# Kernel optimization log

Hardware: AMD Instinct MI355X
Metric: run time of the kernel (lower is better)

The kernel has to match this reference:

```python
import jax, jax.numpy as jnp
import numpy as np
import math

S = 128
EPS = 1e-05

def _rope_seq(x):
    # x: [B, L, 2, s]; rope over dim=1 (sequence), matching torch rope(x, dim=1)
    B, L, two, s = x.shape
    half = s // 2
    pos = jnp.arange(L, dtype=jnp.float32)[:, None]              # [L,1] (one unsqueeze)
    inv_freq = 10000.0 ** (jnp.arange(half, dtype=jnp.float32) / half)
    sinusoid = pos[..., None] * inv_freq[None, None, :]          # [L,1,half]
    sin = jnp.sin(sinusoid)
    cos = jnp.cos(sinusoid)
    x1, x2 = jnp.split(x, 2, axis=-1)
    return jnp.concatenate([x1 * cos - x2 * sin, x2 * cos + x1 * sin], axis=-1)

def setup_inputs() -> dict:
    key = jax.random.key(0)
    ks = jax.random.split(key, 8)
    B, L, D = 8, 1024, 1024
    E = 2 * D
    x = jax.random.normal(ks[0], (B, L, D), dtype=jnp.float32)
    g = jnp.ones((1,), dtype=jnp.float32)
    uv_w = jax.random.normal(ks[1], (2 * E + S, D), dtype=jnp.float32) * 0.02
    gamma = jax.random.uniform(ks[2], (2, S), dtype=jnp.float32)
    beta = jax.random.uniform(ks[3], (2, S), dtype=jnp.float32)
    w_rel = jax.random.uniform(ks[4], (2 * L - 1,), dtype=jnp.float32)
    o_w = jax.random.normal(ks[5], (D, E), dtype=jnp.float32) * 0.02
    res_scale = jnp.ones((D,), dtype=jnp.float32)
    return {"x": x, "g": g, "uv_w": uv_w, "gamma": gamma, "beta": beta,
            "w_rel": w_rel, "o_w": o_w, "res_scale": res_scale}

def reference(x, g, uv_w, gamma, beta, w_rel, o_w, res_scale):
    B, L, D = x.shape
    E = (uv_w.shape[0] - S) // 2
    sqrt_s = math.sqrt(S)
    # ScaleNorm
    norm = jnp.linalg.norm(x, axis=-1, keepdims=True) * (D ** -0.5)
    xn = x / jnp.maximum(norm, EPS) * g
    # gated projection + activation
    uv = jax.nn.silu(xn @ uv_w.T)                               # [B,L,2E+S]
    u = uv[..., :E]
    v = uv[..., E:2 * E]
    base = uv[..., 2 * E:]                                       # [B,L,S]
    base = base[:, :, None, :] * gamma[None, None] + beta        # [B,L,2,S]
    base = _rope_seq(base)
    q = base[:, :, 0]                                            # [B,L,S]
    k = base[:, :, 1]
    qk = jnp.einsum('bis,bjs->bij', q, k)                        # [B,L,L]
    # Toeplitz relative bias: bias[i,j] = w_rel[j - i + L - 1]
    idx = jnp.arange(L)[None, :] - jnp.arange(L)[:, None] + (L - 1)
    qk = qk + w_rel[idx][None]
    kernel = jnp.square(jax.nn.relu(qk / sqrt_s))
    out = u * jnp.einsum('bij,bje->bie', kernel, v)              # [B,L,E]
    out = out @ o_w.T                                            # [B,L,D]
    return x * res_scale + out
```

## Files before the change

### kernel.cpp

```cpp
#include <hip/hip_runtime.h>
#include <hip/hip_bf16.h>
#include <math.h>


typedef __hip_bfloat16 bf16;
using v8s = __attribute__((ext_vector_type(8))) short;
using v4f = __attribute__((ext_vector_type(4))) float;
typedef unsigned short u16;

#define BTCH 8
#define LSEQ 1024
#define DDIM 1024
#define EDIM 2048
#define SDIM 128
#define UVN  4224
#define SLABW 4096
#define BUFW  (4 * SLABW)

__device__ __forceinline__ float ldany(const void* p, size_t i, int bf) {
  return bf ? __bfloat162float(((const bf16*)p)[i]) : ((const float*)p)[i];
}
__device__ __forceinline__ void stany(void* p, size_t i, float v, int bf) {
  if (bf) ((bf16*)p)[i] = __float2bfloat16(v);
  else    ((float*)p)[i] = v;
}
__device__ __forceinline__ u16 f2bf(float x) {
  bf16 b = __float2bfloat16(x);
  return *reinterpret_cast<u16*>(&b);
}
__device__ __forceinline__ float bf2f(u16 u) {
  return __uint_as_float((unsigned)u << 16);
}
__device__ __forceinline__ float silu(float v) {
  return v / (1.0f + __expf(-v));
}

__device__ __forceinline__ void xcd_swz(int& bx, int& by) {
  const int W = gridDim.x;
  const int G = W * gridDim.y;
  const int orig = blockIdx.y * W + blockIdx.x;
  const int nid = (orig & 7) * (G >> 3) + (orig >> 3);
  bx = nid % W;
  by = nid / W;
}

__device__ __forceinline__ void gld16(const u16* g, u16* l) {
  __builtin_amdgcn_global_load_lds(
      (const __attribute__((address_space(1))) void*)g,
      (__attribute__((address_space(3))) void*)l, 16, 0, 0);
}

__device__ __forceinline__ const v8s* swz_rd(const u16* slab, int row, int q) {
  return (const v8s*)(slab + row * 32 + ((q ^ ((row >> 1) & 3)) << 3));
}

__global__ void detect_kernel(const u16* g16, int* flag) {
  *flag = (g16[0] == 0x3F80) ? 1 : 0;
}

__global__ __launch_bounds__(256) void wsplit_kernel(const void* __restrict__ w,
                                                     u16* __restrict__ whi,
                                                     u16* __restrict__ wlo,
                                                     const int* __restrict__ flagp,
                                                     int n) {
  const int bf = *flagp;
  const size_t i = ((size_t)blockIdx.x * 256 + threadIdx.x) * 8;
  if (i >= (size_t)n) return;
  if (bf) {
    *(uint4*)(whi + i) = *(const uint4*)((const u16*)w + i);
  } else {
    const float* wf = (const float*)w;
    float t[8];
    *(float4*)&t[0] = *(const float4*)(wf + i);
    *(float4*)&t[4] = *(const float4*)(wf + i + 4);
    u16 h[8], l[8];
    #pragma unroll
    for (int j = 0; j < 8; j++) {
      h[j] = f2bf(t[j]);
      l[j] = f2bf(t[j] - bf2f(h[j]));
    }
    *(uint4*)(whi + i) = *(uint4*)&h[0];
    *(uint4*)(wlo + i) = *(uint4*)&l[0];
  }
}

__global__ __launch_bounds__(256) void rmsnorm_kernel(const void* __restrict__ x,
                                                      const void* __restrict__ g,
                                                      u16* __restrict__ xnhi,
                                                      u16* __restrict__ xnlo,
                                                      const int* __restrict__ flagp,
                                                      unsigned long long row0) {
  const int bf = *flagp;
  const int m = blockIdx.x;
  const size_t gbase = (row0 + m) * DDIM;
  float ss = 0.f;
  float vals[4];
  #pragma unroll
  for (int i = 0; i < 4; i++) {
    vals[i] = ldany(x, gbase + threadIdx.x + i * 256, bf);
    ss += vals[i] * vals[i];
  }
  #pragma unroll
  for (int o = 32; o > 0; o >>= 1) ss += __shfl_down(ss, o);
  __shared__ float red[5];
  if ((threadIdx.x & 63) == 0) red[threadIdx.x >> 6] = ss;
  __syncthreads();
  if (threadIdx.x == 0) {
    float tot = red[0] + red[1] + red[2] + red[3];
    float rms = sqrtf(tot * (1.0f / DDIM));
    red[4] = ldany(g, 0, bf) / fmaxf(rms, 1e-5f);
  }
  __syncthreads();
  const float scale = red[4];
  #pragma unroll
  for (int i = 0; i < 4; i++) {
    const size_t idx = (size_t)m * DDIM + threadIdx.x + i * 256;
    float v = vals[i] * scale;
    u16 h = f2bf(v);
    xnhi[idx] = h;
    xnlo[idx] = f2bf(v - bf2f(h));
  }
}

__device__ __forceinline__ void mfma_core(u16* __restrict__ sm,
                                          const u16* __restrict__ AhiG,
                                          const u16* __restrict__ AloG, int lda,
                                          const u16* __restrict__ BhiG,
                                          const u16* __restrict__ BloG, int ldb,
                                          int use_blo, int K, v4f acc[4][4]) {
  const int tid = threadIdx.x;
  const int w = tid >> 6, lane = tid & 63, quad = lane >> 4, lr = lane & 15;
  const int wr = w >> 1, wc = w & 1;
  const int sr0 = w * 16 + (lane >> 2);
  const int sch = lane & 3;

  auto stage = [&](int buf, int kk) {
    u16* lbase = sm + buf * BUFW + w * 512;
    #pragma unroll
    for (int c = 0; c < 2; c++) {
      const int r = sr0 + c * 64;
      const int sc = sch ^ ((r >> 1) & 3);
      u16* ld = lbase + c * 2048;
      const size_t oa = (size_t)r * lda + kk + sc * 8;
      const size_t ob = (size_t)r * ldb + kk + sc * 8;
      gld16(AhiG + oa, ld);
      gld16(AloG + oa, ld + SLABW);
      gld16(BhiG + ob, ld + 2 * SLABW);
      if (use_blo) gld16(BloG + ob, ld + 3 * SLABW);
    }
  };

  stage(0, 0);
  __syncthreads();
  int cur = 0;
  for (int k0 = 0; k0 < K; k0 += 32) {
    if (k0 + 32 < K) stage(cur ^ 1, k0 + 32);
    const u16* sA = sm + cur * BUFW;
    v8s aH[4], aL[4], bh[4], bl[4];
    #pragma unroll
    for (int rt = 0; rt < 4; rt++) {
      const int row = wr * 64 + rt * 16 + lr;
      aH[rt] = *swz_rd(sA, row, quad);
      aL[rt] = *swz_rd(sA + SLABW, row, quad);
    }
    #pragma unroll
    for (int ct = 0; ct < 4; ct++) {
      const int brow = wc * 64 + ct * 16 + lr;
      bh[ct] = *swz_rd(sA + 2 * SLABW, brow, quad);
      if (use_blo) bl[ct] = *swz_rd(sA + 3 * SLABW, brow, quad);
    }
    #pragma unroll
    for (int ct = 0; ct < 4; ct++) {
      #pragma unroll
      for (int rt = 0; rt < 4; rt++)
        acc[rt][ct] = __builtin_amdgcn_mfma_f32_16x16x32_bf16(aH[rt], bh[ct], acc[rt][ct], 0, 0, 0);
      #pragma unroll
      for (int rt = 0; rt < 4; rt++)
        acc[rt][ct] = __builtin_amdgcn_mfma_f32_16x16x32_bf16(aL[rt], bh[ct], acc[rt][ct], 0, 0, 0);
      if (use_blo) {
        #pragma unroll
        for (int rt = 0; rt < 4; rt++)
          acc[rt][ct] = __builtin_amdgcn_mfma_f32_16x16x32_bf16(aH[rt], bl[ct], acc[rt][ct], 0, 0, 0);
      }
    }
    __syncthreads();
    cur ^= 1;
  }
}

template <typename F>
__device__ __forceinline__ void epilogue_rows(const v4f acc[4][4], F body) {
  const int tid = threadIdx.x;
  const int w = tid >> 6, lane = tid & 63;
  const int quad = lane >> 4, lr = lane & 15;
  const int wr = w >> 1, wc = w & 1;
  #pragma unroll
  for (int rt = 0; rt < 4; rt++)
    #pragma unroll
    for (int rg = 0; rg < 4; rg++) {
      const int lrow = wr * 64 + rt * 16 + quad * 4 + rg;
      #pragma unroll
      for (int ct = 0; ct < 4; ct++) {
        const int lcol = wc * 64 + ct * 16 + lr;
        body(lrow, lcol, acc[rt][ct][rg]);
      }
    }
}

__global__ __launch_bounds__(256) void gemm_uv_kernel(const u16* __restrict__ xnhi,
                                                      const u16* __restrict__ xnlo,
                                                      const u16* __restrict__ uvwhi,
                                                      const u16* __restrict__ uvwlo,
                                                      float* __restrict__ u,
                                                      u16* __restrict__ vThi,
                                                      u16* __restrict__ vTlo,
                                                      float* __restrict__ base,
                                                      const int* __restrict__ flagp) {
  __shared__ __align__(16) u16 sm[2 * BUFW];
  const int bf = *flagp;
  int bxi, byi;
  xcd_swz(bxi, byi);
  const int bm = byi * 128, bn = bxi * 128;
  v4f acc[4][4];
  #pragma unroll
  for (int rt = 0; rt < 4; rt++)
    #pragma unroll
    for (int ct = 0; ct < 4; ct++) acc[rt][ct] = (v4f){0.f, 0.f, 0.f, 0.f};
  mfma_core(sm, xnhi + (size_t)bm * DDIM, xnlo + (size_t)bm * DDIM, DDIM,
            uvwhi + (size_t)bn * DDIM, uvwlo + (size_t)bn * DDIM, DDIM,
            bf ? 0 : 1, DDIM, acc);

  if (bn < EDIM) {
    epilogue_rows(acc, [&](int lrow, int lcol, float av) {
      u[(size_t)(bm + lrow) * EDIM + bn + lcol] = silu(av);
    });
  } else if (bn < 2 * EDIM) {
    const int z = bm >> 10, l0 = bm & (LSEQ - 1), e0 = bn - EDIM;
    const int tid = threadIdx.x;
    #pragma unroll
    for (int pass = 0; pass < 2; pass++) {
      __syncthreads();
      epilogue_rows(acc, [&](int lrow, int lcol, float av) {
        const float v = silu(av);
        const u16 hh = f2bf(v);
        sm[lcol * 136 + lrow] = pass ? f2bf(v - bf2f(hh)) : hh;
      });
      __syncthreads();
      u16* dst = pass ? vTlo : vThi;
      const int c = tid >> 1, part = tid & 1;
      const uint4* srcp = (const uint4*)(sm + c * 136 + part * 64);
      uint4* dstp = (uint4*)(dst + ((size_t)z * EDIM + e0 + c) * LSEQ + l0 + part * 64);
      #pragma unroll
      for (int j = 0; j < 8; j++) dstp[j] = srcp[j];
    }
  } else {
    epilogue_rows(acc, [&](int lrow, int lcol, float av) {
      base[(size_t)(bm + lrow) * SDIM + (bn - 2 * EDIM) + lcol] = silu(av);
    });
  }
}

__global__ __launch_bounds__(64) void rope_kernel(const float* __restrict__ base,
                                                  const void* __restrict__ gamma,
                                                  const void* __restrict__ beta,
                                                  u16* __restrict__ qhi,
                                                  u16* __restrict__ qlo,
                                                  u16* __restrict__ khi,
                                                  u16* __restrict__ klo,
                                                  const int* __restrict__ flagp) {
  const int bf = *flagp;
  const int m = blockIdx.x;
  const int pos = m & (LSEQ - 1);
  const int j = threadIdx.x;
  double f = pow(10000.0, (double)j / 64.0);
  double ds, dc;
  sincos((double)pos * f, &ds, &dc);
  const float s = (float)ds, c = (float)dc;
  const float b1 = base[(size_t)m * SDIM + j];
  const float b2 = base[(size_t)m * SDIM + 64 + j];
  {
    float x1 = b1 * ldany(gamma, j, bf) + ldany(beta, j, bf);
    float x2 = b2 * ldany(gamma, 64 + j, bf) + ldany(beta, 64 + j, bf);
    float o1 = x1 * c - x2 * s, o2 = x2 * c + x1 * s;
    u16 h1 = f2bf(o1), h2 = f2bf(o2);
    qhi[(size_t)m * SDIM + j] = h1;      qlo[(size_t)m * SDIM + j] = f2bf(o1 - bf2f(h1));
    qhi[(size_t)m * SDIM + 64 + j] = h2; qlo[(size_t)m * SDIM + 64 + j] = f2bf(o2 - bf2f(h2));
  }
  {
    float x1 = b1 * ldany(gamma, SDIM + j, bf) + ldany(beta, SDIM + j, bf);
    float x2 = b2 * ldany(gamma, SDIM + 64 + j, bf) + ldany(beta, SDIM + 64 + j, bf);
    float o1 = x1 * c - x2 * s, o2 = x2 * c + x1 * s;
    u16 h1 = f2bf(o1), h2 = f2bf(o2);
    khi[(size_t)m * SDIM + j] = h1;      klo[(size_t)m * SDIM + j] = f2bf(o1 - bf2f(h1));
    khi[(size_t)m * SDIM + 64 + j] = h2; klo[(size_t)m * SDIM + 64 + j] = f2bf(o2 - bf2f(h2));
  }
}

__global__ __launch_bounds__(256) void gemm_qk_kernel(const u16* __restrict__ qhi,
                                                      const u16* __restrict__ qlo,
                                                      const u16* __restrict__ khi,
                                                      const u16* __restrict__ klo,
                                                      const void* __restrict__ w_rel,
                                                      u16* __restrict__ kerhi,
                                                      u16* __restrict__ kerlo,
                                                      const int* __restrict__ flagp) {
  __shared__ __align__(16) u16 sm[2 * BUFW];
  const int bf = *flagp;
  const int z = blockIdx.z;
  int bxi, byi;
  xcd_swz(bxi, byi);
  const int bm = byi * 128, bn = bxi * 128;
  v4f acc[4][4];
  #pragma unroll
  for (int rt = 0; rt < 4; rt++)
    #pragma unroll
    for (int ct = 0; ct < 4; ct++) acc[rt][ct] = (v4f){0.f, 0.f, 0.f, 0.f};
  const size_t ao = ((size_t)z * LSEQ + bm) * SDIM;
  const size_t bo = ((size_t)z * LSEQ + bn) * SDIM;
  mfma_core(sm, qhi + ao, qlo + ao, SDIM, khi + bo, klo + bo, SDIM, 1, SDIM, acc);
  const float inv_sqrt_s = 0.08838834764831845f;
  epilogue_rows(acc, [&](int lrow, int lcol, float av) {
    const int gi = bm + lrow, gj = bn + lcol;
    float v = av + ldany(w_rel, gj - gi + (LSEQ - 1), bf);
    v = fmaxf(v, 0.f) * inv_sqrt_s;
    v = v * v;
    const u16 hh = f2bf(v);
    const size_t idx = ((size_t)z * LSEQ + gi) * LSEQ + gj;
    kerhi[idx] = hh;
    kerlo[idx] = f2bf(v - bf2f(hh));
  });
}

__global__ __launch_bounds__(256) void gemm_av_kernel(const u16* __restrict__ kerhi,
                                                      const u16* __restrict__ kerlo,
                                                      const u16* __restrict__ vThi,
                                                      const u16* __restrict__ vTlo,
                                                      const float* __restrict__ u,
                                                      u16* __restrict__ out2hi,
                                                      u16* __restrict__ out2lo) {
  __shared__ __align__(16) u16 sm[2 * BUFW];
  const int z = blockIdx.z;
  int bxi, byi;
  xcd_swz(bxi, byi);
  const int bm = byi * 128, bn = bxi * 128;
  v4f acc[4][4];
  #pragma unroll
  for (int rt = 0; rt < 4; rt++)
    #pragma unroll
    for (int ct = 0; ct < 4; ct++) acc[rt][ct] = (v4f){0.f, 0.f, 0.f, 0.f};
  const size_t ao = ((size_t)z * LSEQ + bm) * LSEQ;
  const size_t bo = ((size_t)z * EDIM + bn) * LSEQ;
  mfma_core(sm, kerhi + ao, kerlo + ao, LSEQ, vThi + bo, vTlo + bo, LSEQ,
            1, LSEQ, acc);
  epilogue_rows(acc, [&](int lrow, int lcol, float av) {
    const size_t grow = (size_t)z * LSEQ + bm + lrow;
    const float v = av * u[grow * EDIM + bn + lcol];
    const u16 hh = f2bf(v);
    out2hi[grow * EDIM + bn + lcol] = hh;
    out2lo[grow * EDIM + bn + lcol] = f2bf(v - bf2f(hh));
  });
}

__global__ __launch_bounds__(256) void gemm_out_kernel(const u16* __restrict__ out2hi,
                                                       const u16* __restrict__ out2lo,
                                                       const u16* __restrict__ owhi,
                                                       const u16* __restrict__ owlo,
                                                       const void* __restrict__ x,
                                                       const void* __restrict__ res_scale,
                                                       void* __restrict__ out,
                                                       const int* __restrict__ flagp,
                                                       unsigned long long row0) {
  __shared__ __align__(16) u16 sm[2 * BUFW];
  const int bf = *flagp;
  int bxi, byi;
  xcd_swz(bxi, byi);
  const int bm = byi * 128, bn = bxi * 128;
  v4f acc[4][4];
  #pragma unroll
  for (int rt = 0; rt < 4; rt++)
    #pragma unroll
    for (int ct = 0; ct < 4; ct++) acc[rt][ct] = (v4f){0.f, 0.f, 0.f, 0.f};
  mfma_core(sm, out2hi + (size_t)bm * EDIM, out2lo + (size_t)bm * EDIM, EDIM,
            owhi + (size_t)bn * EDIM, owlo + (size_t)bn * EDIM, EDIM,
            bf ? 0 : 1, EDIM, acc);
  epilogue_rows(acc, [&](int lrow, int lcol, float av) {
    const size_t gidx = (row0 + bm + lrow) * DDIM + bn + lcol;
    float v = av + ldany(x, gidx, bf) * ldany(res_scale, bn + lcol, bf);
    stany(out, gidx, v, bf);
  });
}

extern "C" void kernel_launch(void* const* d_in, const int* in_sizes, int n_in,
                              void* d_out, int out_size, void* d_ws, size_t ws_size,
                              hipStream_t stream) {
  const void* x         = d_in[0];
  const void* g         = d_in[1];
  const void* uv_w      = d_in[2];
  const void* gamma     = d_in[3];
  const void* beta      = d_in[4];
  const void* w_rel     = d_in[5];
  const void* o_w       = d_in[6];
  const void* res_scale = d_in[7];

  char* ws = (char*)d_ws;
  size_t off = 0;
  int* flag = (int*)(ws + off); off += 256;
  u16* uvwhi = (u16*)(ws + off); off += (size_t)UVN * DDIM * 2;
  u16* uvwlo = (u16*)(ws + off); off += (size_t)UVN * DDIM * 2;
  u16* owhi  = (u16*)(ws + off); off += (size_t)DDIM * EDIM * 2;
  u16* owlo  = (u16*)(ws + off); off += (size_t)DDIM * EDIM * 2;

  int nb = 1;
  for (int cand = 8; cand >= 1; cand >>= 1) {
    size_t need = off + (size_t)cand * 35127296ULL;
    if (ws_size >= need) { nb = cand; break; }
  }
  const int rows = nb * LSEQ;

  u16*   xnhi = (u16*)(ws + off); off += (size_t)rows * DDIM * 2;
  u16*   xnlo = (u16*)(ws + off); off += (size_t)rows * DDIM * 2;
  float* u    = (float*)(ws + off); off += (size_t)rows * EDIM * 4;
  float* base = (float*)(ws + off); off += (size_t)rows * SDIM * 4;
  u16*   qhi  = (u16*)(ws + off); off += (size_t)rows * SDIM * 2;
  u16*   qlo  = (u16*)(ws + off); off += (size_t)rows * SDIM * 2;
  u16*   khi  = (u16*)(ws + off); off += (size_t)rows * SDIM * 2;
  u16*   klo  = (u16*)(ws + off); off += (size_t)rows * SDIM * 2;
  u16*   kerhi= (u16*)(ws + off); off += (size_t)nb * LSEQ * LSEQ * 2;
  u16*   kerlo= (u16*)(ws + off); off += (size_t)nb * LSEQ * LSEQ * 2;
  u16*   vThi = (u16*)(ws + off); off += (size_t)nb * EDIM * LSEQ * 2;
  u16*   vTlo = (u16*)(ws + off); off += (size_t)nb * EDIM * LSEQ * 2;
  u16*   o2hi = (u16*)(ws + off); off += (size_t)rows * EDIM * 2;
  u16*   o2lo = (u16*)(ws + off); off += (size_t)rows * EDIM * 2;

  detect_kernel<<<1, 1, 0, stream>>>((const u16*)g, flag);
  wsplit_kernel<<<(UVN * DDIM) / (8 * 256), 256, 0, stream>>>(uv_w, uvwhi, uvwlo,
                                                              flag, UVN * DDIM);
  wsplit_kernel<<<(DDIM * EDIM) / (8 * 256), 256, 0, stream>>>(o_w, owhi, owlo,
                                                               flag, DDIM * EDIM);

  for (int b = 0; b < BTCH / nb; b++) {
    const unsigned long long row0 = (unsigned long long)b * rows;

    rmsnorm_kernel<<<rows, 256, 0, stream>>>(x, g, xnhi, xnlo, flag, row0);
    {
      dim3 grid(UVN / 128, rows / 128);
      gemm_uv_kernel<<<grid, 256, 0, stream>>>(xnhi, xnlo, uvwhi, uvwlo, u,
                                               vThi, vTlo, base, flag);
    }
    rope_kernel<<<rows, 64, 0, stream>>>(base, gamma, beta, qhi, qlo, khi, klo, flag);
    {
      dim3 grid(LSEQ / 128, LSEQ / 128, nb);
      gemm_qk_kernel<<<grid, 256, 0, stream>>>(qhi, qlo, khi, klo, w_rel,
                                               kerhi, kerlo, flag);
    }
    {
      dim3 grid(EDIM / 128, LSEQ / 128, nb);
      gemm_av_kernel<<<grid, 256, 0, stream>>>(kerhi, kerlo, vThi, vTlo, u,
                                               o2hi, o2lo);
    }
    {
      dim3 grid(DDIM / 128, rows / 128);
      gemm_out_kernel<<<grid, 256, 0, stream>>>(o2hi, o2lo, owhi, owlo, x,
                                                res_scale, d_out, flag, row0);
    }
  }
}
```

Before: 676.6 us.

## Use 256x128 tiles with 512-thread blocks for UV and AV GEMMs

Adds a new MFMA main loop that stages a 256-row A tile and a 128-row B tile, run by 8 waves. The UV-projection and kernel-times-V GEMMs switch to it, so each B tile is loaded from global memory half as often and fewer blocks are launched. The transposed-V epilogue becomes four passes, writing each 128-row half through LDS. The XCD swizzle is also generalised to grids whose block count is not a multiple of 8. The new loop stages into a single LDS buffer rather than double-buffering, which may reduce overlap between loads and MFMAs. The larger blocks may also lower occupancy.

```diff
diff --git a/kernel.cpp b/kernel.cpp
--- a/kernel.cpp
+++ b/kernel.cpp
@@ -16,6 +16,8 @@
 #define UVN  4224
 #define SLABW 4096
 #define BUFW  (4 * SLABW)
+#define ASLAB256 8192
+#define BUF256 (2 * ASLAB256 + 2 * SLABW)
 
 __device__ __forceinline__ float ldany(const void* p, size_t i, int bf) {
   return bf ? __bfloat162float(((const bf16*)p)[i]) : ((const float*)p)[i];
@@ -39,7 +41,10 @@
   const int W = gridDim.x;
   const int G = W * gridDim.y;
   const int orig = blockIdx.y * W + blockIdx.x;
-  const int nid = (orig & 7) * (G >> 3) + (orig >> 3);
+  const int xcd = orig & 7;
+  const int q = G >> 3, r = G & 7;
+  const int nid = (xcd < r ? xcd * (q + 1) : r * (q + 1) + (xcd - r) * q)
+                  + (orig >> 3);
   bx = nid % W;
   by = nid / W;
 }
@@ -188,6 +193,76 @@
   }
 }
 
+__device__ __forceinline__ void mfma_core256(u16* __restrict__ sm,
+                                             const u16* __restrict__ AhiG,
+                                             const u16* __restrict__ AloG, int lda,
+                                             const u16* __restrict__ BhiG,
+                                             const u16* __restrict__ BloG, int ldb,
+                                             int use_blo, int K, v4f acc[4][4]) {
+  const int tid = threadIdx.x;
+  const int w = tid >> 6, lane = tid & 63, quad = lane >> 4, lr = lane & 15;
+  const int wr = w >> 1, wc = w & 1;
+  const int rb = w * 16 + (lane >> 2);
+  const int sch = lane & 3;
+  u16* sAhi = sm;
+  u16* sAlo = sm + ASLAB256;
+  u16* sBhi = sm + 2 * ASLAB256;
+  u16* sBlo = sBhi + SLABW;
+
+  auto stage = [&](int kk) {
+    #pragma unroll
+    for (int c = 0; c < 2; c++) {
+      const int r = rb + c * 128;
+      const int sc = sch ^ ((r >> 1) & 3);
+      const size_t oa = (size_t)r * lda + kk + sc * 8;
+      u16* ld = sm + w * 512 + c * 4096;
+      gld16(AhiG + oa, ld);
+      gld16(AloG + oa, ld + ASLAB256);
+    }
+    {
+      const int sc = sch ^ ((rb >> 1) & 3);
+      const size_t ob = (size_t)rb * ldb + kk + sc * 8;
+      gld16(BhiG + ob, sBhi + w * 512);
+      if (use_blo) gld16(BloG + ob, sBlo + w * 512);
+    }
+  };
+
+  stage(0);
+  __syncthreads();
+  for (int k0 = 0; k0 < K; k0 += 32) {
+    v8s aH[4], aL[4], bh[4], bl[4];
+    #pragma unroll
+    for (int rt = 0; rt < 4; rt++) {
+      const int row = wr * 64 + rt * 16 + lr;
+      aH[rt] = *swz_rd(sAhi, row, quad);
+      aL[rt] = *swz_rd(sAlo, row, quad);
+    }
+    #pragma unroll
+    for (int ct = 0; ct < 4; ct++) {
+      const int brow = wc * 64 + ct * 16 + lr;
+      bh[ct] = *swz_rd(sBhi, brow, quad);
+      if (use_blo) bl[ct] = *swz_rd(sBlo, brow, quad);
+    }
+    __syncthreads();
+    if (k0 + 32 < K) stage(k0 + 32);
+    #pragma unroll
+    for (int ct = 0; ct < 4; ct++) {
+      #pragma unroll
+      for (int rt = 0; rt < 4; rt++)
+        acc[rt][ct] = __builtin_amdgcn_mfma_f32_16x16x32_bf16(aH[rt], bh[ct], acc[rt][ct], 0, 0, 0);
+      #pragma unroll
+      for (int rt = 0; rt < 4; rt++)
+        acc[rt][ct] = __builtin_amdgcn_mfma_f32_16x16x32_bf16(aL[rt], bh[ct], acc[rt][ct], 0, 0, 0);
+      if (use_blo) {
+        #pragma unroll
+        for (int rt = 0; rt < 4; rt++)
+          acc[rt][ct] = __builtin_amdgcn_mfma_f32_16x16x32_bf16(aH[rt], bl[ct], acc[rt][ct], 0, 0, 0);
+      }
+    }
+    __syncthreads();
+  }
+}
+
 template <typename F>
 __device__ __forceinline__ void epilogue_rows(const v4f acc[4][4], F body) {
   const int tid = threadIdx.x;
@@ -207,7 +282,7 @@
     }
 }
 
-__global__ __launch_bounds__(256) void gemm_uv_kernel(const u16* __restrict__ xnhi,
+__global__ __launch_bounds__(512) void gemm_uv_kernel(const u16* __restrict__ xnhi,
                                                       const u16* __restrict__ xnlo,
                                                       const u16* __restrict__ uvwhi,
                                                       const u16* __restrict__ uvwlo,
@@ -216,19 +291,19 @@
                                                       u16* __restrict__ vTlo,
                                                       float* __restrict__ base,
                                                       const int* __restrict__ flagp) {
-  __shared__ __align__(16) u16 sm[2 * BUFW];
+  __shared__ __align__(16) u16 sm[BUF256];
   const int bf = *flagp;
   int bxi, byi;
   xcd_swz(bxi, byi);
-  const int bm = byi * 128, bn = bxi * 128;
+  const int bm = byi * 256, bn = bxi * 128;
   v4f acc[4][4];
   #pragma unroll
   for (int rt = 0; rt < 4; rt++)
     #pragma unroll
     for (int ct = 0; ct < 4; ct++) acc[rt][ct] = (v4f){0.f, 0.f, 0.f, 0.f};
-  mfma_core(sm, xnhi + (size_t)bm * DDIM, xnlo + (size_t)bm * DDIM, DDIM,
-            uvwhi + (size_t)bn * DDIM, uvwlo + (size_t)bn * DDIM, DDIM,
-            bf ? 0 : 1, DDIM, acc);
+  mfma_core256(sm, xnhi + (size_t)bm * DDIM, xnlo + (size_t)bm * DDIM, DDIM,
+               uvwhi + (size_t)bn * DDIM, uvwlo + (size_t)bn * DDIM, DDIM,
+               bf ? 0 : 1, DDIM, acc);
 
   if (bn < EDIM) {
     epilogue_rows(acc, [&](int lrow, int lcol, float av) {
@@ -237,21 +312,25 @@
   } else if (bn < 2 * EDIM) {
     const int z = bm >> 10, l0 = bm & (LSEQ - 1), e0 = bn - EDIM;
     const int tid = threadIdx.x;
-    #pragma unroll
-    for (int pass = 0; pass < 2; pass++) {
+    const int wrh = (tid >> 8) & 1;
+    #pragma unroll
+    for (int pass = 0; pass < 4; pass++) {
+      const int h = pass >> 1, p = pass & 1;
       __syncthreads();
-      epilogue_rows(acc, [&](int lrow, int lcol, float av) {
-        const float v = silu(av);
-        const u16 hh = f2bf(v);
-        sm[lcol * 136 + lrow] = pass ? f2bf(v - bf2f(hh)) : hh;
-      });
+      if (wrh == h) {
+        epilogue_rows(acc, [&](int lrow, int lcol, float av) {
+          const float v = silu(av);
+          const u16 hh = f2bf(v);
+          sm[lcol * 136 + (lrow & 127)] = p ? f2bf(v - bf2f(hh)) : hh;
+        });
+      }
       __syncthreads();
-      u16* dst = pass ? vTlo : vThi;
-      const int c = tid >> 1, part = tid & 1;
-      const uint4* srcp = (const uint4*)(sm + c * 136 + part * 64);
-      uint4* dstp = (uint4*)(dst + ((size_t)z * EDIM + e0 + c) * LSEQ + l0 + part * 64);
+      u16* dst = p ? vTlo : vThi;
+      const int c = tid >> 2, part = tid & 3;
+      const uint4* srcp = (const uint4*)(sm + c * 136 + part * 32);
+      uint4* dstp = (uint4*)(dst + ((size_t)z * EDIM + e0 + c) * LSEQ + l0 + h * 128 + part * 32);
       #pragma unroll
-      for (int j = 0; j < 8; j++) dstp[j] = srcp[j];
+      for (int j = 0; j < 4; j++) dstp[j] = srcp[j];
     }
   } else {
     epilogue_rows(acc, [&](int lrow, int lcol, float av) {
@@ -331,18 +410,18 @@
   });
 }
 
-__global__ __launch_bounds__(256) void gemm_av_kernel(const u16* __restrict__ kerhi,
+__global__ __launch_bounds__(512) void gemm_av_kernel(const u16* __restrict__ kerhi,
                                                       const u16* __restrict__ kerlo,
                                                       const u16* __restrict__ vThi,
                                                       const u16* __restrict__ vTlo,
                                                       const float* __restrict__ u,
                                                       u16* __restrict__ out2hi,
                                                       u16* __restrict__ out2lo) {
-  __shared__ __align__(16) u16 sm[2 * BUFW];
+  __shared__ __align__(16) u16 sm[BUF256];
   const int z = blockIdx.z;
   int bxi, byi;
   xcd_swz(bxi, byi);
-  const int bm = byi * 128, bn = bxi * 128;
+  const int bm = byi * 256, bn = bxi * 128;
   v4f acc[4][4];
   #pragma unroll
   for (int rt = 0; rt < 4; rt++)
@@ -350,8 +429,8 @@
     for (int ct = 0; ct < 4; ct++) acc[rt][ct] = (v4f){0.f, 0.f, 0.f, 0.f};
   const size_t ao = ((size_t)z * LSEQ + bm) * LSEQ;
   const size_t bo = ((size_t)z * EDIM + bn) * LSEQ;
-  mfma_core(sm, kerhi + ao, kerlo + ao, LSEQ, vThi + bo, vTlo + bo, LSEQ,
-            1, LSEQ, acc);
+  mfma_core256(sm, kerhi + ao, kerlo + ao, LSEQ, vThi + bo, vTlo + bo, LSEQ,
+               1, LSEQ, acc);
   epilogue_rows(acc, [&](int lrow, int lcol, float av) {
     const size_t grow = (size_t)z * LSEQ + bm + lrow;
     const float v = av * u[grow * EDIM + bn + lcol];
@@ -443,8 +522,8 @@
 
     rmsnorm_kernel<<<rows, 256, 0, stream>>>(x, g, xnhi, xnlo, flag, row0);
     {
-      dim3 grid(UVN / 128, rows / 128);
-      gemm_uv_kernel<<<grid, 256, 0, stream>>>(xnhi, xnlo, uvwhi, uvwlo, u,
+      dim3 grid(UVN / 128, rows / 256);
+      gemm_uv_kernel<<<grid, 512, 0, stream>>>(xnhi, xnlo, uvwhi, uvwlo, u,
                                                vThi, vTlo, base, flag);
     }
     rope_kernel<<<rows, 64, 0, stream>>>(base, gamma, beta, qhi, qlo, khi, klo, flag);
@@ -454,8 +533,8 @@
                                                kerhi, kerlo, flag);
     }
     {
-      dim3 grid(EDIM / 128, LSEQ / 128, nb);
-      gemm_av_kernel<<<grid, 256, 0, stream>>>(kerhi, kerlo, vThi, vTlo, u,
+      dim3 grid(EDIM / 128, LSEQ / 256, nb);
+      gemm_av_kernel<<<grid, 512, 0, stream>>>(kerhi, kerlo, vThi, vTlo, u,
                                                o2hi, o2lo);
     }
     {
```

Measured after the change: 739.4 us. 1.09x slower.
